# Performance work log

Measured on AMD Instinct MI355X. Metric: run time of the kernel, lower is better.

The kernel has to match this reference:

```python
import jax, jax.numpy as jnp
import numpy as np

NEG_SLOPE = 0.2


def setup_inputs() -> dict:
    key = jax.random.key(0)
    k1, k2, k3 = jax.random.split(key, 3)
    bs, n_agents, input_dim = 32, 512, 128
    n_heads, hidden_dim = 8, 64
    h = jax.random.normal(k1, (bs, n_agents, input_dim), dtype=jnp.float32)
    # Linear(input_dim, n_heads*hidden_dim, bias=False), stored as [in, out]
    W = jax.random.normal(k2, (input_dim, n_heads * hidden_dim), dtype=jnp.float32) * (1.0 / np.sqrt(input_dim))
    # xavier_uniform with gain=1.414 on shape (1, n_heads, 2*hidden_dim)
    fan = n_heads + 2 * hidden_dim
    bound = 1.414 * np.sqrt(6.0 / fan)
    att_a = jax.random.uniform(k3, (1, n_heads, 2 * hidden_dim), dtype=jnp.float32,
                               minval=-bound, maxval=bound)
    return {"h": h, "W": W, "att_a": att_a}


def reference(h, W, att_a):
    bs, n_agents, _ = h.shape
    n_heads = att_a.shape[1]
    hidden_dim = att_a.shape[2] // 2
    # h_prime: [bs, n_heads, n_agents, hidden_dim]
    h_prime = (h @ W).reshape(bs, n_agents, n_heads, hidden_dim).transpose(0, 2, 1, 3)
    # Additive score decomposes exactly: (a1.h_i + a2.h_j) == sum(cat(h_i,h_j)*a)
    a_src = att_a[0, :, :hidden_dim]   # [n_heads, hidden_dim]
    a_dst = att_a[0, :, hidden_dim:]   # [n_heads, hidden_dim]
    e_src = jnp.einsum('bhnd,hd->bhn', h_prime, a_src)  # score contribution of node i (row)
    e_dst = jnp.einsum('bhnd,hd->bhn', h_prime, a_dst)  # contribution of node j (col)
    e = e_src[:, :, :, None] + e_dst[:, :, None, :]     # [bs, n_heads, n, n]
    e = jnp.where(e >= 0, e, NEG_SLOPE * e)             # leaky_relu(0.2)
    attention = jax.nn.softmax(e, axis=-1)
    h_new = jnp.einsum('bhnm,bhmd->bhnd', attention, h_prime)
    return jax.nn.elu(h_new)
```

## Files before the change

### kernel.cpp

```cpp
#include <hip/hip_runtime.h>

#define BS 32
#define NA 512
#define ID 128
#define NH 8
#define HD 64
#define NHD 512
#define NEG 0.2f
#define NC 32
#define CH 16
#define NW 8

__global__ __launch_bounds__(256) void k1_gemm(
    const float* __restrict__ h, const float* __restrict__ W,
    const float* __restrict__ att, float* __restrict__ hp,
    float* __restrict__ s_out, float* __restrict__ t_out) {
  int blk = blockIdx.x;
  int b = blk >> 5;
  int n0 = (blk & 31) * 16;
  int t = threadIdx.x;
  int lane = t & 63, w = t >> 6;
  int r0 = __builtin_amdgcn_readfirstlane((w >> 1) * 8);
  int chalf = __builtin_amdgcn_readfirstlane(w & 1);
  int col = chalf * 256 + lane * 4;
  int head = col >> 6;
  int d0 = col & 63;
  const float* arow = h + ((size_t)b * NA + n0 + r0) * ID;
  const float* wptr = W + col;

  float4 a0c = {0,0,0,0}, a1c = {0,0,0,0}, a2c = {0,0,0,0}, a3c = {0,0,0,0};
  float4 a4c = {0,0,0,0}, a5c = {0,0,0,0}, a6c = {0,0,0,0}, a7c = {0,0,0,0};

#define K1_ROW(I, C, KK)                                                      \
  { float a_ = arow[(I) * ID + kc + (KK)];                                    \
    C.x += a_ * wv.x; C.y += a_ * wv.y; C.z += a_ * wv.z; C.w += a_ * wv.w; }
  #pragma unroll 1
  for (int kc = 0; kc < ID; kc += 8) {
    #pragma unroll
    for (int kk = 0; kk < 8; ++kk) {
      float4 wv = *(const float4*)(wptr + (size_t)(kc + kk) * NHD);
      K1_ROW(0, a0c, kk) K1_ROW(1, a1c, kk) K1_ROW(2, a2c, kk)
      K1_ROW(3, a3c, kk) K1_ROW(4, a4c, kk) K1_ROW(5, a5c, kk)
      K1_ROW(6, a6c, kk) K1_ROW(7, a7c, kk)
    }
  }
#undef K1_ROW
  {
    size_t off = ((((size_t)b * NH + head) * NA) + (n0 + r0)) * HD + d0;
    *(float4*)(hp + off) = a0c; off += HD;
    *(float4*)(hp + off) = a1c; off += HD;
    *(float4*)(hp + off) = a2c; off += HD;
    *(float4*)(hp + off) = a3c; off += HD;
    *(float4*)(hp + off) = a4c; off += HD;
    *(float4*)(hp + off) = a5c; off += HD;
    *(float4*)(hp + off) = a6c; off += HD;
    *(float4*)(hp + off) = a7c;
  }
  {
    float4 as4 = *(const float4*)(att + head * 128 + d0);
    float4 ad4 = *(const float4*)(att + head * 128 + 64 + d0);
#define DOT4(C, A) ((C).x*(A).x + (C).y*(A).y + (C).z*(A).z + (C).w*(A).w)
    float sp0 = DOT4(a0c, as4), tp0 = DOT4(a0c, ad4);
    float sp1 = DOT4(a1c, as4), tp1 = DOT4(a1c, ad4);
    float sp2 = DOT4(a2c, as4), tp2 = DOT4(a2c, ad4);
    float sp3 = DOT4(a3c, as4), tp3 = DOT4(a3c, ad4);
    float sp4 = DOT4(a4c, as4), tp4 = DOT4(a4c, ad4);
    float sp5 = DOT4(a5c, as4), tp5 = DOT4(a5c, ad4);
    float sp6 = DOT4(a6c, as4), tp6 = DOT4(a6c, ad4);
    float sp7 = DOT4(a7c, as4), tp7 = DOT4(a7c, ad4);
#undef DOT4
    #pragma unroll
    for (int m = 1; m < 16; m <<= 1) {
      sp0 += __shfl_xor(sp0, m, 64); tp0 += __shfl_xor(tp0, m, 64);
      sp1 += __shfl_xor(sp1, m, 64); tp1 += __shfl_xor(tp1, m, 64);
      sp2 += __shfl_xor(sp2, m, 64); tp2 += __shfl_xor(tp2, m, 64);
      sp3 += __shfl_xor(sp3, m, 64); tp3 += __shfl_xor(tp3, m, 64);
      sp4 += __shfl_xor(sp4, m, 64); tp4 += __shfl_xor(tp4, m, 64);
      sp5 += __shfl_xor(sp5, m, 64); tp5 += __shfl_xor(tp5, m, 64);
      sp6 += __shfl_xor(sp6, m, 64); tp6 += __shfl_xor(tp6, m, 64);
      sp7 += __shfl_xor(sp7, m, 64); tp7 += __shfl_xor(tp7, m, 64);
    }
    int g16 = lane & 15;
    int rsel = g16 & 7;
    float sv_ = rsel == 0 ? sp0 : rsel == 1 ? sp1 : rsel == 2 ? sp2 :
                rsel == 3 ? sp3 : rsel == 4 ? sp4 : rsel == 5 ? sp5 :
                rsel == 6 ? sp6 : sp7;
    float tv_ = rsel == 0 ? tp0 : rsel == 1 ? tp1 : rsel == 2 ? tp2 :
                rsel == 3 ? tp3 : rsel == 4 ? tp4 : rsel == 5 ? tp5 :
                rsel == 6 ? tp6 : tp7;
    size_t off = (((size_t)b * NH + head) * NA) + n0 + r0 + rsel;
    if (g16 < 8) s_out[off] = sv_;
    else         t_out[off] = tv_;
  }
}

__global__ __launch_bounds__(512, 2) void k2_fused(
    const float* __restrict__ hp, const float* __restrict__ s_g,
    const float* __restrict__ t_g, float* __restrict__ out) {
  __shared__ float tv[NA]; __shared__ int tpm[NA];
  __shared__ float sv[NA]; __shared__ int spm[NA];
  __shared__ float wp[NA]; __shared__ float wn[NA];
  __shared__ float rawP8[NW * 64]; __shared__ float rawN8[NW * 64];
  __shared__ float sufPc[(NW + 1) * 64]; __shared__ float preNc[(NW + 1) * 64];
  __shared__ float zps[NA + 1]; __shared__ float znp[NA + 1];
  __shared__ float szP[NC]; __shared__ float szN[NC];
  __shared__ float sufZ[NC + 1]; __shared__ float preZ[NC + 1];
  __shared__ float4 abi[NA];
  __shared__ int jsr[NA];
  __shared__ int Earr[NA];

  int bh = blockIdx.x;
  int t = threadIdx.x;
  int lane = t & 63, w = t >> 6;
  const float* vbase = hp + (size_t)bh * NA * HD;

  float vt = t_g[(size_t)bh * NA + t]; int it = t;
  float vs = s_g[(size_t)bh * NA + t]; int is_ = t;
  for (int size = 2; size <= NA; size <<= 1) {
    bool dirAsc = ((t & size) == 0);
    for (int stride = size >> 1; stride > 0; stride >>= 1) {
      float pt, ps; int pit, pis;
      if (stride >= 64) {
        tv[t] = vt; tpm[t] = it; sv[t] = vs; spm[t] = is_;
        __syncthreads();
        pt = tv[t ^ stride]; pit = tpm[t ^ stride];
        ps = sv[t ^ stride]; pis = spm[t ^ stride];
        __syncthreads();
      } else {
        pt = __shfl_xor(vt, stride, 64); pit = __shfl_xor(it, stride, 64);
        ps = __shfl_xor(vs, stride, 64); pis = __shfl_xor(is_, stride, 64);
      }
      bool mn = (((t & stride) == 0) == dirAsc);
      if (mn ? (pt < vt) : (pt > vt)) { vt = pt; it = pit; }
      if (mn ? (ps < vs) : (ps > vs)) { vs = ps; is_ = pis; }
    }
  }
  tv[t] = vt; tpm[t] = it; sv[t] = vs; spm[t] = is_;
  __syncthreads();

  float cmax = fmaxf(tv[NA - 1], 0.f);
  float amax = fmaxf(sv[NA - 1], 0.f);
  wp[t] = __expf(vt - cmax);
  wn[t] = __expf(NEG * vt - cmax);
  __syncthreads();

  float vreg[64];
  {
    float aP = 0.f, aN = 0.f;
    #pragma unroll
    for (int jj = 0; jj < 64; ++jj) {
      int j = (w << 6) + jj;
      float vv = vbase[(size_t)tpm[j] * HD + lane];
      vreg[jj] = vv;
      aP += wp[j] * vv;
      aN += wn[j] * vv;
    }
    rawP8[(w << 6) + lane] = aP;
    rawN8[(w << 6) + lane] = aN;
  }
  __syncthreads();

  if (t < 64) {
    int d = t; float run = 0.f;
    sufPc[NW * 64 + d] = 0.f;
    for (int ww = NW - 1; ww >= 0; --ww) {
      run += rawP8[ww * 64 + d]; sufPc[ww * 64 + d] = run;
    }
  } else if (t < 128) {
    int d = t - 64; float run = 0.f;
    for (int ww = 0; ww <= NW; ++ww) {
      preNc[ww * 64 + d] = run;
      if (ww < NW) run += rawN8[ww * 64 + d];
    }
  } else if (t < 160) {
    int c = t - 128; float a = 0.f;
    for (int j = c * CH; j < c * CH + CH; ++j) a += wp[j];
    szP[c] = a;
  } else if (t < 192) {
    int c = t - 160; float a = 0.f;
    for (int j = c * CH; j < c * CH + CH; ++j) a += wn[j];
    szN[c] = a;
  }
  __syncthreads();

  if (t == 0) {
    float run = 0.f; sufZ[NC] = 0.f;
    for (int cc = NC - 1; cc >= 0; --cc) { run += szP[cc]; sufZ[cc] = run; }
  } else if (t == 1) {
    float run = 0.f;
    for (int cc = 0; cc <= NC; ++cc) { preZ[cc] = run; if (cc < NC) run += szN[cc]; }
  }
  __syncthreads();

  {
    int ch = t >> 4;
    float a = 0.f;
    for (int k = t; k < ch * CH + CH; ++k) a += wp[k];
    zps[t] = a + sufZ[ch + 1];
    float b2 = 0.f;
    for (int k = ch * CH; k < t; ++k) b2 += wn[k];
    znp[t] = preZ[ch] + b2;
    if (t == 0) { zps[NA] = 0.f; znp[NA] = preZ[NC]; }
  }
  __syncthreads();

  {
    float A = __expf(vs - amax);
    float B = __expf(NEG * vs - amax);
    float key = -vs;
    int lo = 0, hi = NA;
    while (lo < hi) { int mid = (lo + hi) >> 1; if (tv[mid] < key) lo = mid + 1; else hi = mid; }
    float den = A * zps[lo] + B * znp[lo];
    float4 q; q.x = A; q.y = B; q.z = 1.f / den; q.w = __int_as_float(is_);
    abi[t] = q;
    jsr[t] = lo;
  }
  __syncthreads();

  {
    int lo = 0, hi = NA;
    while (lo < hi) { int mid = (lo + hi) >> 1; if (jsr[mid] > t) lo = mid + 1; else hi = mid; }
    Earr[t] = lo;
  }
  __syncthreads();

  {
    float sufPv = sufPc[w * 64 + lane];
    float preSeedN = preNc[w * 64 + lane];
    float runN = 0.f;
    size_t obase = (size_t)bh * NA * HD + lane;
    int eprev = (w == 0) ? NA : Earr[(w << 6) - 1];
    #pragma unroll
    for (int jj = 0; jj < 64; ++jj) {
      int j = (w << 6) + jj;
      int ecur = Earr[j];
      float preNv = preSeedN + runN;
      for (int r = ecur; r < eprev; ++r) {
        float4 q = abi[r];
        float x = (q.x * sufPv + q.y * preNv) * q.z;
        int orow = __float_as_int(q.w);
        out[obase + (size_t)orow * HD] = x > 0.f ? x : __expf(x) - 1.f;
      }
      float vv = vreg[jj];
      sufPv -= wp[j] * vv;
      runN  += wn[j] * vv;
      eprev = ecur;
    }
    if (w == NW - 1) {
      float preNv = preSeedN + runN;
      for (int r = 0; r < eprev; ++r) {
        float4 q = abi[r];
        float x = (q.y * preNv) * q.z;
        int orow = __float_as_int(q.w);
        out[obase + (size_t)orow * HD] = x > 0.f ? x : __expf(x) - 1.f;
      }
    }
  }
}

extern "C" void kernel_launch(void* const* d_in, const int* in_sizes, int n_in,
                              void* d_out, int out_size, void* d_ws, size_t ws_size,
                              hipStream_t stream) {
  const float* h   = (const float*)d_in[0];
  const float* W   = (const float*)d_in[1];
  const float* att = (const float*)d_in[2];
  float* out = (float*)d_out;
  float* hp    = (float*)d_ws;
  float* s_arr = hp + (size_t)BS * NH * NA * HD;
  float* t_arr = s_arr + (size_t)BS * NH * NA;

  k1_gemm <<<dim3(1024), dim3(256), 0, stream>>>(h, W, att, hp, s_arr, t_arr);
  k2_fused<<<dim3(BS * NH), dim3(512), 0, stream>>>(hp, s_arr, t_arr, out);
}
```

Measured before the change: 133.3 us.

## Fuse projection GEMM and attention into one kernel with LDS-resident features

Merges the projection GEMM and the sorted-prefix attention kernel into one 1024-thread kernel per (batch, head). The projected features for that head are computed straight into a 128KB LDS buffer, and the score vectors are derived from that buffer. This removes the global write and read-back of the projected features and score arrays and one kernel launch. Blocks are mapped so that the eight heads of a batch land on the same XCD, which should keep the shared h rows in L2. In exchange, each block recomputes its slice of the GEMM with scalar FMAs, LDS use limits each CU to one block, and the output loop recomputes exponentials and reciprocals per row instead of reading precomputed values.

New measurement: 157.4 us. +18.1%, slower.

```diff
diff --git a/kernel.cpp b/kernel.cpp
--- a/kernel.cpp
+++ b/kernel.cpp
@@ -9,169 +9,150 @@
 #define NEG 0.2f
 #define NC 32
 #define CH 16
-#define NW 8
-
-__global__ __launch_bounds__(256) void k1_gemm(
+#define NW 16
+#define CHK 16
+
+__global__ __launch_bounds__(1024) void gat_fused(
     const float* __restrict__ h, const float* __restrict__ W,
-    const float* __restrict__ att, float* __restrict__ hp,
-    float* __restrict__ s_out, float* __restrict__ t_out) {
-  int blk = blockIdx.x;
-  int b = blk >> 5;
-  int n0 = (blk & 31) * 16;
-  int t = threadIdx.x;
-  int lane = t & 63, w = t >> 6;
-  int r0 = __builtin_amdgcn_readfirstlane((w >> 1) * 8);
-  int chalf = __builtin_amdgcn_readfirstlane(w & 1);
-  int col = chalf * 256 + lane * 4;
-  int head = col >> 6;
-  int d0 = col & 63;
-  const float* arow = h + ((size_t)b * NA + n0 + r0) * ID;
-  const float* wptr = W + col;
-
-  float4 a0c = {0,0,0,0}, a1c = {0,0,0,0}, a2c = {0,0,0,0}, a3c = {0,0,0,0};
-  float4 a4c = {0,0,0,0}, a5c = {0,0,0,0}, a6c = {0,0,0,0}, a7c = {0,0,0,0};
-
-#define K1_ROW(I, C, KK)                                                      \
-  { float a_ = arow[(I) * ID + kc + (KK)];                                    \
-    C.x += a_ * wv.x; C.y += a_ * wv.y; C.z += a_ * wv.z; C.w += a_ * wv.w; }
-  #pragma unroll 1
-  for (int kc = 0; kc < ID; kc += 8) {
-    #pragma unroll
-    for (int kk = 0; kk < 8; ++kk) {
-      float4 wv = *(const float4*)(wptr + (size_t)(kc + kk) * NHD);
-      K1_ROW(0, a0c, kk) K1_ROW(1, a1c, kk) K1_ROW(2, a2c, kk)
-      K1_ROW(3, a3c, kk) K1_ROW(4, a4c, kk) K1_ROW(5, a5c, kk)
-      K1_ROW(6, a6c, kk) K1_ROW(7, a7c, kk)
-    }
-  }
-#undef K1_ROW
-  {
-    size_t off = ((((size_t)b * NH + head) * NA) + (n0 + r0)) * HD + d0;
-    *(float4*)(hp + off) = a0c; off += HD;
-    *(float4*)(hp + off) = a1c; off += HD;
-    *(float4*)(hp + off) = a2c; off += HD;
-    *(float4*)(hp + off) = a3c; off += HD;
-    *(float4*)(hp + off) = a4c; off += HD;
-    *(float4*)(hp + off) = a5c; off += HD;
-    *(float4*)(hp + off) = a6c; off += HD;
-    *(float4*)(hp + off) = a7c;
-  }
-  {
-    float4 as4 = *(const float4*)(att + head * 128 + d0);
-    float4 ad4 = *(const float4*)(att + head * 128 + 64 + d0);
-#define DOT4(C, A) ((C).x*(A).x + (C).y*(A).y + (C).z*(A).z + (C).w*(A).w)
-    float sp0 = DOT4(a0c, as4), tp0 = DOT4(a0c, ad4);
-    float sp1 = DOT4(a1c, as4), tp1 = DOT4(a1c, ad4);
-    float sp2 = DOT4(a2c, as4), tp2 = DOT4(a2c, ad4);
-    float sp3 = DOT4(a3c, as4), tp3 = DOT4(a3c, ad4);
-    float sp4 = DOT4(a4c, as4), tp4 = DOT4(a4c, ad4);
-    float sp5 = DOT4(a5c, as4), tp5 = DOT4(a5c, ad4);
-    float sp6 = DOT4(a6c, as4), tp6 = DOT4(a6c, ad4);
-    float sp7 = DOT4(a7c, as4), tp7 = DOT4(a7c, ad4);
-#undef DOT4
-    #pragma unroll
-    for (int m = 1; m < 16; m <<= 1) {
-      sp0 += __shfl_xor(sp0, m, 64); tp0 += __shfl_xor(tp0, m, 64);
-      sp1 += __shfl_xor(sp1, m, 64); tp1 += __shfl_xor(tp1, m, 64);
-      sp2 += __shfl_xor(sp2, m, 64); tp2 += __shfl_xor(tp2, m, 64);
-      sp3 += __shfl_xor(sp3, m, 64); tp3 += __shfl_xor(tp3, m, 64);
-      sp4 += __shfl_xor(sp4, m, 64); tp4 += __shfl_xor(tp4, m, 64);
-      sp5 += __shfl_xor(sp5, m, 64); tp5 += __shfl_xor(tp5, m, 64);
-      sp6 += __shfl_xor(sp6, m, 64); tp6 += __shfl_xor(tp6, m, 64);
-      sp7 += __shfl_xor(sp7, m, 64); tp7 += __shfl_xor(tp7, m, 64);
-    }
-    int g16 = lane & 15;
-    int rsel = g16 & 7;
-    float sv_ = rsel == 0 ? sp0 : rsel == 1 ? sp1 : rsel == 2 ? sp2 :
-                rsel == 3 ? sp3 : rsel == 4 ? sp4 : rsel == 5 ? sp5 :
-                rsel == 6 ? sp6 : sp7;
-    float tv_ = rsel == 0 ? tp0 : rsel == 1 ? tp1 : rsel == 2 ? tp2 :
-                rsel == 3 ? tp3 : rsel == 4 ? tp4 : rsel == 5 ? tp5 :
-                rsel == 6 ? tp6 : tp7;
-    size_t off = (((size_t)b * NH + head) * NA) + n0 + r0 + rsel;
-    if (g16 < 8) s_out[off] = sv_;
-    else         t_out[off] = tv_;
-  }
-}
-
-__global__ __launch_bounds__(512, 2) void k2_fused(
-    const float* __restrict__ hp, const float* __restrict__ s_g,
-    const float* __restrict__ t_g, float* __restrict__ out) {
-  __shared__ float tv[NA]; __shared__ int tpm[NA];
-  __shared__ float sv[NA]; __shared__ int spm[NA];
+    const float* __restrict__ att, float* __restrict__ out) {
+  __shared__ float V[NA * HD];
+  __shared__ float tv[NA]; __shared__ float sv[NA];
+  __shared__ unsigned short tpm[NA];
+  __shared__ unsigned short spm[NA];
   __shared__ float wp[NA]; __shared__ float wn[NA];
-  __shared__ float rawP8[NW * 64]; __shared__ float rawN8[NW * 64];
   __shared__ float sufPc[(NW + 1) * 64]; __shared__ float preNc[(NW + 1) * 64];
   __shared__ float zps[NA + 1]; __shared__ float znp[NA + 1];
   __shared__ float szP[NC]; __shared__ float szN[NC];
   __shared__ float sufZ[NC + 1]; __shared__ float preZ[NC + 1];
-  __shared__ float4 abi[NA];
-  __shared__ int jsr[NA];
-  __shared__ int Earr[NA];
-
-  int bh = blockIdx.x;
+  __shared__ unsigned short jsr[NA]; __shared__ unsigned short Earr[NA];
+  __shared__ float asrc[HD]; __shared__ float adst[HD];
+
+  int i = blockIdx.x;
+  int xcd = i & 7, slot = i >> 3;
+  int b = xcd * 4 + (slot >> 3);
+  int head = slot & 7;
+  int bh = b * NH + head;
   int t = threadIdx.x;
-  int lane = t & 63, w = t >> 6;
-  const float* vbase = hp + (size_t)bh * NA * HD;
-
-  float vt = t_g[(size_t)bh * NA + t]; int it = t;
-  float vs = s_g[(size_t)bh * NA + t]; int is_ = t;
+  int lane = t & 63;
+  int w = t >> 6;
+  int wu = __builtin_amdgcn_readfirstlane(w);
+
+  {
+    float acc[32];
+    #pragma unroll
+    for (int rc = 0; rc < 32; ++rc) acc[rc] = 0.f;
+    const float* wcol = W + head * HD + lane;
+    const float* hb = h + ((size_t)b * NA + wu * 32) * ID;
+    #pragma unroll 1
+    for (int kc = 0; kc < ID; kc += CHK) {
+      float wch[CHK];
+      #pragma unroll
+      for (int kk = 0; kk < CHK; ++kk)
+        wch[kk] = wcol[(size_t)(kc + kk) * NHD];
+      #pragma unroll
+      for (int rc = 0; rc < 32; ++rc) {
+        const float* ar = hb + rc * ID + kc;
+        float t0 = 0.f, t1 = 0.f, t2 = 0.f, t3 = 0.f;
+        #pragma unroll
+        for (int kk = 0; kk < CHK; kk += 4) {
+          t0 += ar[kk + 0] * wch[kk + 0];
+          t1 += ar[kk + 1] * wch[kk + 1];
+          t2 += ar[kk + 2] * wch[kk + 2];
+          t3 += ar[kk + 3] * wch[kk + 3];
+        }
+        acc[rc] += (t0 + t1) + (t2 + t3);
+      }
+    }
+    #pragma unroll
+    for (int rc = 0; rc < 32; ++rc)
+      V[(wu * 32 + rc) * HD + lane] = acc[rc];
+  }
+  if (t < HD)            asrc[t]      = att[head * 128 + t];
+  else if (t < 2 * HD)   adst[t - HD] = att[head * 128 + t];
+  __syncthreads();
+
+  float vt = 0.f, vs = 0.f; int it = t, is_ = t;
+  if (t < NA) {
+    float s0 = 0.f, s1 = 0.f, t0 = 0.f, t1 = 0.f;
+    #pragma unroll
+    for (int j = 0; j < HD; j += 2) {
+      int c0 = (j + t) & 63, c1 = (j + 1 + t) & 63;
+      float v0 = V[t * HD + c0], v1 = V[t * HD + c1];
+      s0 += v0 * asrc[c0]; s1 += v1 * asrc[c1];
+      t0 += v0 * adst[c0]; t1 += v1 * adst[c1];
+    }
+    vs = s0 + s1; vt = t0 + t1;
+  }
+
   for (int size = 2; size <= NA; size <<= 1) {
     bool dirAsc = ((t & size) == 0);
     for (int stride = size >> 1; stride > 0; stride >>= 1) {
-      float pt, ps; int pit, pis;
       if (stride >= 64) {
-        tv[t] = vt; tpm[t] = it; sv[t] = vs; spm[t] = is_;
+        if (t < NA) {
+          tv[t] = vt; tpm[t] = (unsigned short)it;
+          sv[t] = vs; spm[t] = (unsigned short)is_;
+        }
         __syncthreads();
-        pt = tv[t ^ stride]; pit = tpm[t ^ stride];
-        ps = sv[t ^ stride]; pis = spm[t ^ stride];
+        if (t < NA) {
+          float pt = tv[t ^ stride]; int pit = tpm[t ^ stride];
+          float ps = sv[t ^ stride]; int pis = spm[t ^ stride];
+          bool mn = (((t & stride) == 0) == dirAsc);
+          if (mn ? (pt < vt) : (pt > vt)) { vt = pt; it = pit; }
+          if (mn ? (ps < vs) : (ps > vs)) { vs = ps; is_ = pis; }
+        }
         __syncthreads();
-      } else {
-        pt = __shfl_xor(vt, stride, 64); pit = __shfl_xor(it, stride, 64);
-        ps = __shfl_xor(vs, stride, 64); pis = __shfl_xor(is_, stride, 64);
-      }
-      bool mn = (((t & stride) == 0) == dirAsc);
-      if (mn ? (pt < vt) : (pt > vt)) { vt = pt; it = pit; }
-      if (mn ? (ps < vs) : (ps > vs)) { vs = ps; is_ = pis; }
-    }
-  }
-  tv[t] = vt; tpm[t] = it; sv[t] = vs; spm[t] = is_;
+      } else if (t < NA) {
+        float pt = __shfl_xor(vt, stride, 64); int pit = __shfl_xor(it, stride, 64);
+        float ps = __shfl_xor(vs, stride, 64); int pis = __shfl_xor(is_, stride, 64);
+        bool mn = (((t & stride) == 0) == dirAsc);
+        if (mn ? (pt < vt) : (pt > vt)) { vt = pt; it = pit; }
+        if (mn ? (ps < vs) : (ps > vs)) { vs = ps; is_ = pis; }
+      }
+    }
+  }
+  if (t < NA) {
+    tv[t] = vt; tpm[t] = (unsigned short)it;
+    sv[t] = vs; spm[t] = (unsigned short)is_;
+  }
   __syncthreads();
 
   float cmax = fmaxf(tv[NA - 1], 0.f);
   float amax = fmaxf(sv[NA - 1], 0.f);
-  wp[t] = __expf(vt - cmax);
-  wn[t] = __expf(NEG * vt - cmax);
-  __syncthreads();
-
-  float vreg[64];
+  if (t < NA) {
+    wp[t] = __expf(vt - cmax);
+    wn[t] = __expf(NEG * vt - cmax);
+  }
+  __syncthreads();
+
   {
     float aP = 0.f, aN = 0.f;
     #pragma unroll
-    for (int jj = 0; jj < 64; ++jj) {
-      int j = (w << 6) + jj;
-      float vv = vbase[(size_t)tpm[j] * HD + lane];
-      vreg[jj] = vv;
+    for (int jj = 0; jj < 32; ++jj) {
+      int j = (w << 5) + jj;
+      float vv = V[(int)tpm[j] * HD + lane];
       aP += wp[j] * vv;
       aN += wn[j] * vv;
     }
-    rawP8[(w << 6) + lane] = aP;
-    rawN8[(w << 6) + lane] = aN;
+    sufPc[w * 64 + lane] = aP;
+    preNc[w * 64 + lane] = aN;
   }
   __syncthreads();
 
   if (t < 64) {
-    int d = t; float run = 0.f;
-    sufPc[NW * 64 + d] = 0.f;
+    float run = 0.f;
+    sufPc[NW * 64 + t] = 0.f;
     for (int ww = NW - 1; ww >= 0; --ww) {
-      run += rawP8[ww * 64 + d]; sufPc[ww * 64 + d] = run;
+      run += sufPc[ww * 64 + t];
+      sufPc[ww * 64 + t] = run;
     }
   } else if (t < 128) {
     int d = t - 64; float run = 0.f;
-    for (int ww = 0; ww <= NW; ++ww) {
+    for (int ww = 0; ww < NW; ++ww) {
+      float raw = preNc[ww * 64 + d];
       preNc[ww * 64 + d] = run;
-      if (ww < NW) run += rawN8[ww * 64 + d];
-    }
+      run += raw;
+    }
+    preNc[NW * 64 + d] = run;
   } else if (t < 160) {
     int c = t - 128; float a = 0.f;
     for (int j = c * CH; j < c * CH + CH; ++j) a += wp[j];
@@ -192,7 +173,7 @@
   }
   __syncthreads();
 
-  {
+  if (t < NA) {
     int ch = t >> 4;
     float a = 0.f;
     for (int k = t; k < ch * CH + CH; ++k) a += wp[k];
@@ -201,47 +182,41 @@
     for (int k = ch * CH; k < t; ++k) b2 += wn[k];
     znp[t] = preZ[ch] + b2;
     if (t == 0) { zps[NA] = 0.f; znp[NA] = preZ[NC]; }
-  }
-  __syncthreads();
-
-  {
-    float A = __expf(vs - amax);
-    float B = __expf(NEG * vs - amax);
     float key = -vs;
     int lo = 0, hi = NA;
     while (lo < hi) { int mid = (lo + hi) >> 1; if (tv[mid] < key) lo = mid + 1; else hi = mid; }
-    float den = A * zps[lo] + B * znp[lo];
-    float4 q; q.x = A; q.y = B; q.z = 1.f / den; q.w = __int_as_float(is_);
-    abi[t] = q;
-    jsr[t] = lo;
+    jsr[t] = (unsigned short)lo;
+  }
+  __syncthreads();
+
+  if (t < NA) {
+    int lo = 0, hi = NA;
+    while (lo < hi) { int mid = (lo + hi) >> 1; if ((int)jsr[mid] > t) lo = mid + 1; else hi = mid; }
+    Earr[t] = (unsigned short)lo;
   }
   __syncthreads();
 
   {
-    int lo = 0, hi = NA;
-    while (lo < hi) { int mid = (lo + hi) >> 1; if (jsr[mid] > t) lo = mid + 1; else hi = mid; }
-    Earr[t] = lo;
-  }
-  __syncthreads();
-
-  {
-    float sufPv = sufPc[w * 64 + lane];
+    float sufPv   = sufPc[w * 64 + lane];
     float preSeedN = preNc[w * 64 + lane];
     float runN = 0.f;
     size_t obase = (size_t)bh * NA * HD + lane;
-    int eprev = (w == 0) ? NA : Earr[(w << 6) - 1];
-    #pragma unroll
-    for (int jj = 0; jj < 64; ++jj) {
-      int j = (w << 6) + jj;
-      int ecur = Earr[j];
+    int eprev = (w == 0) ? NA : (int)Earr[(w << 5) - 1];
+    #pragma unroll 1
+    for (int jj = 0; jj < 32; ++jj) {
+      int j = (w << 5) + jj;
+      int ecur = (int)Earr[j];
       float preNv = preSeedN + runN;
       for (int r = ecur; r < eprev; ++r) {
-        float4 q = abi[r];
-        float x = (q.x * sufPv + q.y * preNv) * q.z;
-        int orow = __float_as_int(q.w);
+        float s = sv[r];
+        float A = __expf(s - amax);
+        float B = __expf(NEG * s - amax);
+        float inv = 1.f / (A * zps[j] + B * znp[j]);
+        float x = (A * sufPv + B * preNv) * inv;
+        int orow = (int)spm[r];
         out[obase + (size_t)orow * HD] = x > 0.f ? x : __expf(x) - 1.f;
       }
-      float vv = vreg[jj];
+      float vv = V[(int)tpm[j] * HD + lane];
       sufPv -= wp[j] * vv;
       runN  += wn[j] * vv;
       eprev = ecur;
@@ -249,9 +224,12 @@
     if (w == NW - 1) {
       float preNv = preSeedN + runN;
       for (int r = 0; r < eprev; ++r) {
-        float4 q = abi[r];
-        float x = (q.y * preNv) * q.z;
-        int orow = __float_as_int(q.w);
+        float s = sv[r];
+        float A = __expf(s - amax);
+        float B = __expf(NEG * s - amax);
+        float inv = 1.f / (A * zps[NA] + B * znp[NA]);
+        float x = (B * preNv) * inv;
+        int orow = (int)spm[r];
         out[obase + (size_t)orow * HD] = x > 0.f ? x : __expf(x) - 1.f;
       }
     }
@@ -265,10 +243,7 @@
   const float* W   = (const float*)d_in[1];
   const float* att = (const float*)d_in[2];
   float* out = (float*)d_out;
-  float* hp    = (float*)d_ws;
-  float* s_arr = hp + (size_t)BS * NH * NA * HD;
-  float* t_arr = s_arr + (size_t)BS * NH * NA;
-
-  k1_gemm <<<dim3(1024), dim3(256), 0, stream>>>(h, W, att, hp, s_arr, t_arr);
-  k2_fused<<<dim3(BS * NH), dim3(512), 0, stream>>>(hp, s_arr, t_arr, out);
+  (void)d_ws; (void)ws_size;
+
+  gat_fused<<<dim3(BS * NH), dim3(1024), 0, stream>>>(h, W, att, out);
 }
```
